# Optimization experiments

Hardware: AMD Instinct MI355X
Metric: run time of the kernel (lower is better)

The kernel has to match this reference:

```python
import jax, jax.numpy as jnp
import numpy as np

GRID_SIZE = 5
K = 3  # spline order
WIDTH = [512, 1024, 1024, 1024, 256]
BATCH = 4096


def make_grid(in_dim):
    # pykan-style extended uniform grid on [-1, 1]: G + 2K + 1 knots per input dim
    h = 2.0 / GRID_SIZE
    pts = jnp.arange(-K, GRID_SIZE + K + 1, dtype=jnp.float32) * h - 1.0
    return jnp.tile(pts[None, :], (in_dim, 1))


def bspline_basis(x, grid):
    # Cox-de Boor recursion. x: [B, in], grid: [in, G+2K+1] -> basis [B, in, G+K]
    xe = x[..., None]
    b = ((xe >= grid[:, :-1]) & (xe < grid[:, 1:])).astype(x.dtype)  # degree 0: [B, in, G+2K]
    for d in range(1, K + 1):
        left = (xe - grid[:, :-(d + 1)]) / (grid[:, d:-1] - grid[:, :-(d + 1)]) * b[..., :-1]
        right = (grid[:, d + 1:] - xe) / (grid[:, d + 1:] - grid[:, 1:-d]) * b[..., 1:]
        b = left + right
    return b


def kan_layer(x, grid, coef, scale_base, scale_sp):
    # out_j = sum_i scale_base[i,j]*silu(x_i) + scale_sp[i,j]*sum_g coef[i,j,g]*B_g(x_i)
    basis = bspline_basis(x, grid)                                   # [B, in, G+K]
    base = jnp.einsum('bi,io->bo', jax.nn.silu(x), scale_base)
    spline = jnp.einsum('big,iog->bo', basis, coef * scale_sp[:, :, None])
    return base + spline


def setup_inputs() -> dict:
    key = jax.random.key(0)
    n_layers = len(WIDTH) - 1
    keys = jax.random.split(key, 2 + 2 * n_layers)
    inp = {
        'inputs_y': jax.random.normal(keys[0], (BATCH, 256), dtype=jnp.float32) * 0.5,
        'inputs_u': jax.random.normal(keys[1], (BATCH, 256), dtype=jnp.float32) * 0.5,
    }
    for l, (din, dout) in enumerate(zip(WIDTH[:-1], WIDTH[1:])):
        inp[f'coef{l}'] = jax.random.normal(keys[2 + 2 * l], (din, dout, GRID_SIZE + K), dtype=jnp.float32) * (0.1 / np.sqrt(din))
        inp[f'sb{l}'] = jax.random.normal(keys[3 + 2 * l], (din, dout), dtype=jnp.float32) * (1.0 / np.sqrt(din))
        inp[f'ss{l}'] = jnp.ones((din, dout), dtype=jnp.float32)
        inp[f'grid{l}'] = make_grid(din)
    return inp


def reference(inputs_y, inputs_u,
              coef0, sb0, ss0, grid0,
              coef1, sb1, ss1, grid1,
              coef2, sb2, ss2, grid2,
              coef3, sb3, ss3, grid3):
    x = jnp.concatenate([inputs_y.astype(jnp.float32), inputs_u.astype(jnp.float32)], axis=-1)
    layers = [(grid0, coef0, sb0, ss0), (grid1, coef1, sb1, ss1),
              (grid2, coef2, sb2, ss2), (grid3, coef3, sb3, ss3)]
    for g, c, sb, ss in layers:
        x = kan_layer(x, g, c, sb, ss)
    return x
```

## Files before the change

### kernel.cpp

```cpp
#include <hip/hip_runtime.h>
#include <cstdint>
#include <cstddef>

typedef _Float16 f16;
typedef _Float16 f16x4 __attribute__((ext_vector_type(4)));
typedef _Float16 f16x8 __attribute__((ext_vector_type(8)));
typedef float f32x4 __attribute__((ext_vector_type(4)));

__device__ __forceinline__ void gl2lds16(const void* g, void* l) {
  __builtin_amdgcn_global_load_lds(
      (const __attribute__((address_space(1))) void*)(uintptr_t)g,
      (__attribute__((address_space(3))) void*)(uintptr_t)l,
      16, 0, 0);
}

__global__ __launch_bounds__(256) void kan_prep2(
    const float* __restrict__ coef, const float* __restrict__ sb,
    const float* __restrict__ ss, f16* __restrict__ Wt,
    int out, int K9)
{
  __shared__ float s_sb[32][32];
  __shared__ float s_ss[32][32];
  __shared__ f16 s_w[32][288];
  const int t  = threadIdx.x;
  const int o0 = blockIdx.x * 32, i0 = blockIdx.y * 32;

  {
    int il = t >> 3, oc = (t & 7) * 4;
    float4 vb = *(const float4*)(sb + (size_t)(i0 + il) * out + o0 + oc);
    float4 vs = *(const float4*)(ss + (size_t)(i0 + il) * out + o0 + oc);
    s_sb[il][oc + 0] = vb.x; s_sb[il][oc + 1] = vb.y;
    s_sb[il][oc + 2] = vb.z; s_sb[il][oc + 3] = vb.w;
    s_ss[il][oc + 0] = vs.x; s_ss[il][oc + 1] = vs.y;
    s_ss[il][oc + 2] = vs.z; s_ss[il][oc + 3] = vs.w;
  }
  __syncthreads();

#pragma unroll
  for (int j = 0; j < 8; ++j) {
    int f  = j * 256 + t;
    int il = f >> 6, c = f & 63;
    int ol = c >> 1, gh = (c & 1) * 4;
    float4 v = *(const float4*)(coef + ((size_t)(i0 + il) * out + (o0 + ol)) * 8 + gh);
    float ssv = s_ss[il][ol];
    f16* dst = &s_w[ol][il * 9 + 1 + gh];
    dst[0] = (f16)(v.x * ssv); dst[1] = (f16)(v.y * ssv);
    dst[2] = (f16)(v.z * ssv); dst[3] = (f16)(v.w * ssv);
  }
#pragma unroll
  for (int j = 0; j < 4; ++j) {
    int e = j * 256 + t; int il = e >> 5, ol = e & 31;
    s_w[ol][il * 9] = (f16)s_sb[il][ol];
  }
  __syncthreads();

  {
    int o = t >> 3, part = t & 7;
    f16* dst = Wt + (size_t)(o0 + o) * K9 + (size_t)i0 * 9 + part * 36;
    const f16* src = &s_w[o][part * 36];
#pragma unroll
    for (int q = 0; q < 9; ++q)
      *(f16x4*)(dst + q * 4) = *(const f16x4*)(src + q * 4);
  }
}

__global__ __launch_bounds__(256) void kan_feat(
    const float* __restrict__ X, f16* __restrict__ F,
    int shift, int K9, int iBase)
{
  int idx = blockIdx.x * 256 + threadIdx.x;
  int b  = idx >> shift;
  int ii = idx & ((1 << shift) - 1);
  float x = X[idx];

  float sig  = 1.0f / (1.0f + __expf(-x));
  float silu = x * sig;

  float t[12];
#pragma unroll
  for (int j = 0; j < 12; ++j) t[j] = (float)(j - 3) * 0.4f - 1.0f;
  float b0[11];
#pragma unroll
  for (int j = 0; j < 11; ++j)
    b0[j] = (x >= t[j] && x < t[j + 1]) ? 1.0f : 0.0f;
  float b1[10];
#pragma unroll
  for (int j = 0; j < 10; ++j)
    b1[j] = (x - t[j]) * 2.5f * b0[j] + (t[j + 2] - x) * 2.5f * b0[j + 1];
  float b2[9];
#pragma unroll
  for (int j = 0; j < 9; ++j)
    b2[j] = (x - t[j]) * 1.25f * b1[j] + (t[j + 3] - x) * 1.25f * b1[j + 1];
  float b3[8];
#pragma unroll
  for (int j = 0; j < 8; ++j)
    b3[j] = (x - t[j]) * (1.0f / 1.2f) * b2[j] +
            (t[j + 4] - x) * (1.0f / 1.2f) * b2[j + 1];

  f16* o = F + (size_t)b * K9 + (size_t)(iBase + ii) * 9;
  o[0] = (f16)silu;
#pragma unroll
  for (int g = 0; g < 8; ++g) o[1 + g] = (f16)b3[g];
}

template <int SPLITK>
__global__ __launch_bounds__(256, 2) void kan_gemm(
    const f16* __restrict__ A, const f16* __restrict__ Bt,
    float* __restrict__ C, int N, int K)
{
  __shared__ __align__(16) f16 lds[4][8192];
  const int tid   = threadIdx.x;
  const int lane  = tid & 63;
  const int w     = tid >> 6;
  const int waveM = w >> 1, waveN = w & 1;
  const int l16   = lane & 15, quad = lane >> 4;
  const size_t mBase = (size_t)blockIdx.y * 128;
  const size_t nBase = (size_t)blockIdx.x * 128;
  const int kChunk = K / SPLITK;
  const int k0     = blockIdx.z * kChunk;
  const int kSteps = kChunk >> 5;

  const f16* gA[2]; int lA[2];
  const f16* gB[2]; int lB[2];
#pragma unroll
  for (int r = 0; r < 2; ++r) {
    int g = r * 256 + tid, row = g >> 2;
    int cs = (g & 3) ^ ((row >> 1) & 3);
    gA[r] = A + (mBase + row) * (size_t)K + k0 + cs * 8;
    gB[r] = Bt + (nBase + row) * (size_t)K + k0 + cs * 8;
    lA[r] = (r * 256 + (tid & ~63)) * 8;
    lB[r] = 4096 + lA[r];
  }

  f32x4 acc[4][4] = {};

#pragma unroll
  for (int p = 0; p < 3; ++p) {
    f16* b = lds[p];
    int kk = p * 32;
#pragma unroll
    for (int r = 0; r < 2; ++r) {
      gl2lds16(gA[r] + kk, b + lA[r]);
      gl2lds16(gB[r] + kk, b + lB[r]);
    }
  }

  for (int s = 0; s < kSteps; ++s) {
    if (s < kSteps - 2)       asm volatile("s_waitcnt vmcnt(8)" ::: "memory");
    else if (s == kSteps - 2) asm volatile("s_waitcnt vmcnt(4)" ::: "memory");
    else                      asm volatile("s_waitcnt vmcnt(0)" ::: "memory");
    __builtin_amdgcn_s_barrier();

    if (s + 3 < kSteps) {
      int kk = (s + 3) * 32;
      f16* b = lds[(s + 3) & 3];
#pragma unroll
      for (int r = 0; r < 2; ++r) {
        gl2lds16(gA[r] + kk, b + lA[r]);
        gl2lds16(gB[r] + kk, b + lB[r]);
      }
    }

    const f16* buf = lds[s & 3];
    f16x8 af[4], bf[4];
#pragma unroll
    for (int mi = 0; mi < 4; ++mi) {
      int row = waveM * 64 + mi * 16 + l16;
      af[mi] = *(const f16x8*)(buf + row * 32 + (quad ^ ((row >> 1) & 3)) * 8);
    }
#pragma unroll
    for (int ni = 0; ni < 4; ++ni) {
      int col = waveN * 64 + ni * 16 + l16;
      bf[ni] = *(const f16x8*)(buf + 4096 + col * 32 + (quad ^ ((col >> 1) & 3)) * 8);
    }
#pragma unroll
    for (int mi = 0; mi < 4; ++mi)
#pragma unroll
      for (int ni = 0; ni < 4; ++ni)
        acc[mi][ni] = __builtin_amdgcn_mfma_f32_16x16x32_f16(
            af[mi], bf[ni], acc[mi][ni], 0, 0, 0);
  }

#pragma unroll
  for (int mi = 0; mi < 4; ++mi) {
    size_t row = mBase + waveM * 64 + mi * 16 + quad * 4;
#pragma unroll
    for (int ni = 0; ni < 4; ++ni) {
      size_t col = nBase + waveN * 64 + ni * 16 + l16;
#pragma unroll
      for (int r = 0; r < 4; ++r)
        unsafeAtomicAdd(C + (row + r) * N + col, acc[mi][ni][r]);
    }
  }
}

extern "C" void kernel_launch(void* const* d_in, const int* in_sizes, int n_in,
                              void* d_out, int out_size, void* d_ws, size_t ws_size,
                              hipStream_t stream)
{
  const float* y = (const float*)d_in[0];
  const float* u = (const float*)d_in[1];
  const float* coef[4]; const float* sb[4]; const float* ss[4];
  for (int l = 0; l < 4; ++l) {
    coef[l] = (const float*)d_in[2 + 4 * l];
    sb[l]   = (const float*)d_in[3 + 4 * l];
    ss[l]   = (const float*)d_in[4 + 4 * l];
  }
  char* ws = (char*)d_ws;
  f16*   Wt   = (f16*)(ws);
  f16*   F    = (f16*)(ws + 18874368);
  float* actA = (float*)(ws + 18874368 + 75497472);
  float* actB = (float*)(ws + 18874368 + 75497472 + 16777216);
  float* out  = (float*)d_out;
  const size_t actBytes = (size_t)4096 * 1024 * 4;

  kan_prep2<<<dim3(32, 16), 256, 0, stream>>>(coef[0], sb[0], ss[0], Wt, 1024, 4608);
  kan_feat<<<4096 * 256 / 256, 256, 0, stream>>>(y, F, 8, 4608, 0);
  kan_feat<<<4096 * 256 / 256, 256, 0, stream>>>(u, F, 8, 4608, 256);
  hipMemsetAsync(actA, 0, actBytes, stream);
  kan_gemm<2><<<dim3(8, 32, 2), 256, 0, stream>>>(F, Wt, actA, 1024, 4608);

  kan_prep2<<<dim3(32, 32), 256, 0, stream>>>(coef[1], sb[1], ss[1], Wt, 1024, 9216);
  kan_feat<<<4096 * 1024 / 256, 256, 0, stream>>>(actA, F, 10, 9216, 0);
  hipMemsetAsync(actB, 0, actBytes, stream);
  kan_gemm<2><<<dim3(8, 32, 2), 256, 0, stream>>>(F, Wt, actB, 1024, 9216);

  kan_prep2<<<dim3(32, 32), 256, 0, stream>>>(coef[2], sb[2], ss[2], Wt, 1024, 9216);
  kan_feat<<<4096 * 1024 / 256, 256, 0, stream>>>(actB, F, 10, 9216, 0);
  hipMemsetAsync(actA, 0, actBytes, stream);
  kan_gemm<2><<<dim3(8, 32, 2), 256, 0, stream>>>(F, Wt, actA, 1024, 9216);

  kan_prep2<<<dim3(8, 32), 256, 0, stream>>>(coef[3], sb[3], ss[3], Wt, 256, 9216);
  kan_feat<<<4096 * 1024 / 256, 256, 0, stream>>>(actA, F, 10, 9216, 0);
  hipMemsetAsync(d_out, 0, (size_t)out_size * sizeof(float), stream);
  kan_gemm<8><<<dim3(2, 32, 8), 256, 0, stream>>>(F, Wt, out, 256, 9216);
}
```

Baseline: 620.1 us.

## Load GEMM operands directly from global memory instead of staging through LDS

Drops the 4-stage LDS ring buffer fed by global_load_lds, along with its waitcnt/barrier pipeline. Each wave now loads its A and B MFMA fragments straight from global memory into registers, and the loop is unrolled by 2. This removes LDS traffic and block-wide barriers. In exchange, operands shared across waves are fetched redundantly from global/L2, there is no explicit prefetch depth, and each lane reads only 16 bytes per row, a poorly coalesced pattern.

```diff
diff --git a/kernel.cpp b/kernel.cpp
--- a/kernel.cpp
+++ b/kernel.cpp
@@ -6,13 +6,6 @@
 typedef _Float16 f16x4 __attribute__((ext_vector_type(4)));
 typedef _Float16 f16x8 __attribute__((ext_vector_type(8)));
 typedef float f32x4 __attribute__((ext_vector_type(4)));
-
-__device__ __forceinline__ void gl2lds16(const void* g, void* l) {
-  __builtin_amdgcn_global_load_lds(
-      (const __attribute__((address_space(1))) void*)(uintptr_t)g,
-      (__attribute__((address_space(3))) void*)(uintptr_t)l,
-      16, 0, 0);
-}
 
 __global__ __launch_bounds__(256) void kan_prep2(
     const float* __restrict__ coef, const float* __restrict__ sb,
@@ -108,7 +101,6 @@
     const f16* __restrict__ A, const f16* __restrict__ Bt,
     float* __restrict__ C, int N, int K)
 {
-  __shared__ __align__(16) f16 lds[4][8192];
   const int tid   = threadIdx.x;
   const int lane  = tid & 63;
   const int w     = tid >> 6;
@@ -120,58 +112,28 @@
   const int k0     = blockIdx.z * kChunk;
   const int kSteps = kChunk >> 5;
 
-  const f16* gA[2]; int lA[2];
-  const f16* gB[2]; int lB[2];
+  const f16* pA[4]; const f16* pB[4];
 #pragma unroll
-  for (int r = 0; r < 2; ++r) {
-    int g = r * 256 + tid, row = g >> 2;
-    int cs = (g & 3) ^ ((row >> 1) & 3);
-    gA[r] = A + (mBase + row) * (size_t)K + k0 + cs * 8;
-    gB[r] = Bt + (nBase + row) * (size_t)K + k0 + cs * 8;
-    lA[r] = (r * 256 + (tid & ~63)) * 8;
-    lB[r] = 4096 + lA[r];
-  }
+  for (int mi = 0; mi < 4; ++mi)
+    pA[mi] = A + (mBase + waveM * 64 + mi * 16 + l16) * (size_t)K + k0 + quad * 8;
+#pragma unroll
+  for (int ni = 0; ni < 4; ++ni)
+    pB[ni] = Bt + (nBase + waveN * 64 + ni * 16 + l16) * (size_t)K + k0 + quad * 8;
 
   f32x4 acc[4][4] = {};
 
-#pragma unroll
-  for (int p = 0; p < 3; ++p) {
-    f16* b = lds[p];
-    int kk = p * 32;
-#pragma unroll
-    for (int r = 0; r < 2; ++r) {
-      gl2lds16(gA[r] + kk, b + lA[r]);
-      gl2lds16(gB[r] + kk, b + lB[r]);
-    }
-  }
-
+#pragma unroll 2
   for (int s = 0; s < kSteps; ++s) {
-    if (s < kSteps - 2)       asm volatile("s_waitcnt vmcnt(8)" ::: "memory");
-    else if (s == kSteps - 2) asm volatile("s_waitcnt vmcnt(4)" ::: "memory");
-    else                      asm volatile("s_waitcnt vmcnt(0)" ::: "memory");
-    __builtin_amdgcn_s_barrier();
-
-    if (s + 3 < kSteps) {
-      int kk = (s + 3) * 32;
-      f16* b = lds[(s + 3) & 3];
-#pragma unroll
-      for (int r = 0; r < 2; ++r) {
-        gl2lds16(gA[r] + kk, b + lA[r]);
-        gl2lds16(gB[r] + kk, b + lB[r]);
-      }
-    }
-
-    const f16* buf = lds[s & 3];
     f16x8 af[4], bf[4];
 #pragma unroll
     for (int mi = 0; mi < 4; ++mi) {
-      int row = waveM * 64 + mi * 16 + l16;
-      af[mi] = *(const f16x8*)(buf + row * 32 + (quad ^ ((row >> 1) & 3)) * 8);
+      af[mi] = *(const f16x8*)pA[mi];
+      pA[mi] += 32;
     }
 #pragma unroll
     for (int ni = 0; ni < 4; ++ni) {
-      int col = waveN * 64 + ni * 16 + l16;
-      bf[ni] = *(const f16x8*)(buf + 4096 + col * 32 + (quad ^ ((col >> 1) & 3)) * 8);
+      bf[ni] = *(const f16x8*)pB[ni];
+      pB[ni] += 32;
     }
 #pragma unroll
     for (int mi = 0; mi < 4; ++mi)
```

Result: slower. 1.135 ms (+83.0%).
